# Kernel optimization log

Measured on AMD Instinct MI355X. Metric: run time of the kernel, lower is better.

Reference implementation:

```python
import jax, jax.numpy as jnp
import numpy as np

B, HGRID, WGRID = 4, 32, 32
L = 1 + HGRID * WGRID          # cls token + spatial tokens
INPUT_DIM = 512
HEAD_DIM = 512
N_HEAD = 8
QKV_DIM = HEAD_DIM * N_HEAD    # 4096


def pos_embed_2d(h, w, C, dtype):
    """Standard 2D sinusoidal positional embedding, shape (h*w, C)."""
    d = C // 4
    omega = 1.0 / (10000.0 ** (jnp.arange(d, dtype=jnp.float32) / d))
    ey = jnp.arange(h, dtype=jnp.float32)[:, None] * omega      # (h, d)
    ex = jnp.arange(w, dtype=jnp.float32)[:, None] * omega      # (w, d)
    emb_y = jnp.concatenate([jnp.sin(ey), jnp.cos(ey)], -1)     # (h, 2d)
    emb_x = jnp.concatenate([jnp.sin(ex), jnp.cos(ex)], -1)     # (w, 2d)
    emb = jnp.concatenate([
        jnp.broadcast_to(emb_y[:, None, :], (h, w, 2 * d)),
        jnp.broadcast_to(emb_x[None, :, :], (h, w, 2 * d)),
    ], -1)                                                       # (h, w, C)
    return emb.reshape(h * w, C).astype(dtype)


def setup_inputs() -> dict:
    key = jax.random.key(0)
    ks = jax.random.split(key, 16)
    s = 0.02
    inp = {
        "x": jax.random.normal(ks[0], (B, L, INPUT_DIM), dtype=jnp.float32),
        # Q/K/V linear: weight (out, in) as in torch Linear, bias zeros (per _init_bias)
        "Wq": jax.random.normal(ks[1], (QKV_DIM, INPUT_DIM), jnp.float32) * s,
        "bq": jnp.zeros((QKV_DIM,), jnp.float32),
        "Wk": jax.random.normal(ks[2], (QKV_DIM, INPUT_DIM), jnp.float32) * s,
        "bk": jnp.zeros((QKV_DIM,), jnp.float32),
        "Wv": jax.random.normal(ks[3], (QKV_DIM, INPUT_DIM), jnp.float32) * s,
        "bv": jnp.zeros((QKV_DIM,), jnp.float32),
        # 1x1 conv poolers: weight (out_ch, in_ch) = (HEAD_DIM, HEAD_DIM)
        "Wpq": jax.random.normal(ks[4], (HEAD_DIM, HEAD_DIM), jnp.float32) * s,
        "bpq": jax.random.normal(ks[5], (HEAD_DIM,), jnp.float32) * s,
        "Wpk": jax.random.normal(ks[6], (HEAD_DIM, HEAD_DIM), jnp.float32) * s,
        "bpk": jax.random.normal(ks[7], (HEAD_DIM,), jnp.float32) * s,
        "Wpv": jax.random.normal(ks[8], (HEAD_DIM, HEAD_DIM), jnp.float32) * s,
        "bpv": jax.random.normal(ks[9], (HEAD_DIM,), jnp.float32) * s,
        # dispatcher linear: (INPUT_DIM, QKV_DIM)
        "Wd": jax.random.normal(ks[10], (INPUT_DIM, QKV_DIM), jnp.float32) * s,
        "bd": jax.random.normal(ks[11], (INPUT_DIM,), jnp.float32) * s,
        "h": HGRID,
        "w": WGRID,
    }
    return inp


def _pool(t, Wp, bp):
    """AttentionPooler with kernel=1/stride=1: pointwise conv on spatial tokens,
    cls token passed through unchanged. t: (B, n_head, L, head_dim)."""
    cls_tok = t[:, :, :1, :]
    sp = jnp.einsum('bnlc,oc->bnlo', t[:, :, 1:, :], Wp) + bp
    return jnp.concatenate([cls_tok, sp], axis=2)


def reference(x, Wq, bq, Wk, bk, Wv, bv, Wpq, bpq, Wpk, bpk, Wpv, bpv, Wd, bd, h, w):
    Bs, Ls, _ = x.shape

    def proj(Wt, bt):
        y = jnp.einsum('bli,oi->blo', x, Wt) + bt
        return y.reshape(Bs, Ls, N_HEAD, HEAD_DIM).transpose(0, 2, 1, 3)  # (B,nh,L,hd)

    Q = proj(Wq, bq)
    K = proj(Wk, bk)
    V = proj(Wv, bv)

    PQ = _pool(Q, Wpq, bpq)
    PK = _pool(K, Wpk, bpk)
    PV = _pool(V, Wpv, bpv)

    # relative positional encoding added to pooled Q's spatial tokens
    emb = pos_embed_2d(h, w, HEAD_DIM, PQ.dtype)                 # (h*w, hd)
    PQ = jnp.concatenate([PQ[:, :, :1, :], PQ[:, :, 1:, :] + emb], axis=2)

    scale = 1.0 / jnp.sqrt(jnp.asarray(HEAD_DIM, PQ.dtype))
    logits = jnp.einsum('bnqc,bnkc->bnqk', PQ, PK) * scale
    attn = jax.nn.softmax(logits, axis=-1)
    sa = jnp.einsum('bnqk,bnkc->bnqc', attn, PV)

    # skip connection on spatial tokens only (cls row excluded)
    sa = jnp.concatenate([sa[:, :, :1, :], sa[:, :, 1:, :] + Q[:, :, 1:, :]], axis=2)

    stacked = sa.transpose(0, 2, 1, 3).reshape(Bs, Ls, QKV_DIM)
    out = jnp.einsum('blq,oq->blo', stacked, Wd) + bd
    return out
```

## Files before the change

kernel.cpp:

```cpp
#include <hip/hip_runtime.h>


typedef unsigned short u16;
typedef __attribute__((ext_vector_type(8))) short short8;
typedef __attribute__((ext_vector_type(4))) float floatx4;
typedef __attribute__((ext_vector_type(4))) unsigned short us4;

__device__ __forceinline__ u16 f2bf(float f) {
  union { float f; unsigned u; } x; x.f = f;
  unsigned r = (x.u + 0x7fffu + ((x.u >> 16) & 1u)) >> 16;
  return (u16)r;
}
__device__ __forceinline__ float bf2f(u16 u) {
  union { unsigned u; float f; } x; x.u = ((unsigned)u) << 16;
  return x.f;
}

__device__ __forceinline__ void gld_lds16(const void* g, void* l) {
  __builtin_amdgcn_global_load_lds(
      (const __attribute__((address_space(1))) void*)g,
      (__attribute__((address_space(3))) void*)l, 16, 0, 0);
}

struct CvtArgs { const float* src[8]; u16* dst[8]; int n4[8]; };

__global__ __launch_bounds__(256) void cvt_all(CvtArgs a, int total4, float* __restrict__ e) {
  int t = blockIdx.x * 256 + threadIdx.x;
  if (t >= total4) {
    int et = (t - total4) * 4;
    if (et >= 1024 * 512) return;
#pragma unroll
    for (int u = 0; u < 4; ++u) {
      int idx = et + u;
      int c = idx & 511, sp = idx >> 9;
      int y = sp >> 5, xg = sp & 31;
      int j = c & 127, seg = c >> 7;
      float omega = expf(-(float)j * (9.210340371976184f / 128.f));
      float arg = (float)((seg < 2) ? y : xg) * omega;
      e[idx] = (seg & 1) ? cosf(arg) : sinf(arg);
    }
    return;
  }
#pragma unroll
  for (int s = 0; s < 8; ++s) {
    if (t < a.n4[s]) {
      const float* sp = a.src[s] + (long)t * 4;
      u16* dp = a.dst[s] + (long)t * 4;
      float4 v = *(const float4*)sp;
      dp[0] = f2bf(v.x); dp[1] = f2bf(v.y); dp[2] = f2bf(v.z); dp[3] = f2bf(v.w);
      return;
    }
    t -= a.n4[s];
  }
}

__global__ __launch_bounds__(256) void cls_all(
    const u16* __restrict__ Q, const u16* __restrict__ K, const u16* __restrict__ V,
    u16* __restrict__ PQ, u16* __restrict__ PK, u16* __restrict__ PVt) {
  int t = blockIdx.x * 256 + threadIdx.x;
  int bn = t >> 9, c = t & 511;
  long o = (long)bn * 1025 * 512 + c;
  PQ[o] = Q[o];
  PK[o] = K[o];
  PVt[((long)bn * 512 + c) * 1088] = V[o];
}

__global__ __launch_bounds__(256) void s_edge(const u16* __restrict__ PQ,
                                              const u16* __restrict__ PK,
                                              u16* __restrict__ S, int nh) {
  int flat = blockIdx.x;
  int head, seg;
  if (nh == 32) {
    int xcd = flat & 7, s = flat >> 3;
    head = xcd + 8 * (s >> 2);
    seg = s & 3;
  } else {
    head = flat >> 2;
    seg = flat & 3;
  }
  const u16* pq = PQ + (long)head * 1025 * 512;
  const u16* pk = PK + (long)head * 1025 * 512;
  u16* sh = S + (long)head * 1025 * 1088;
#pragma unroll
  for (int i = 0; i < 3; ++i) {
    int local = i * 256 + (int)threadIdx.x;
    if (local >= 513) continue;
    int e = seg * 513 + local;
    if (e >= 2049) continue;
    int q, kv;
    if (e < 1025) { q = 1024; kv = e; }
    else { q = e - 1025; kv = 1024; }
    const u16* a = pq + (long)q * 512;
    const u16* b = pk + (long)kv * 512;
    float acc = 0.f;
    for (int k8 = 0; k8 < 64; ++k8) {
      short8 av = *(const short8*)(a + k8 * 8);
      short8 bv = *(const short8*)(b + k8 * 8);
#pragma unroll
      for (int u = 0; u < 8; ++u) acc += bf2f((u16)av[u]) * bf2f((u16)bv[u]);
    }
    sh[(long)q * 1088 + kv] = f2bf(acc * 0.04419417382415922f);
  }
}

__global__ __launch_bounds__(256) void softmax_rows(u16* __restrict__ S) {
  int flat = blockIdx.x;
  int xcd = flat & 7, s0 = flat >> 3;
  int zi = s0 / 257, blk = s0 - zi * 257;
  int head = xcd + 8 * zi;
  int wv = threadIdx.x >> 6, lane = threadIdx.x & 63;
  int row_i = blk * 4 + wv;
  if (row_i > 1024) return;
  u16* row = S + ((long)head * 1025 + row_i) * 1088;
  float v[16];
  float mx = -1e30f;
#pragma unroll
  for (int i = 0; i < 4; ++i) {
    us4 p = *(const us4*)(row + i * 256 + lane * 4);
#pragma unroll
    for (int e = 0; e < 4; ++e) { v[i * 4 + e] = bf2f(p[e]); mx = fmaxf(mx, v[i * 4 + e]); }
  }
  float e1024 = (lane == 0) ? bf2f(row[1024]) : -1e30f;
  mx = fmaxf(mx, e1024);
  for (int o = 32; o > 0; o >>= 1) mx = fmaxf(mx, __shfl_xor(mx, o, 64));
  float s = 0.f;
#pragma unroll
  for (int i = 0; i < 16; ++i) { v[i] = __expf(v[i] - mx); s += v[i]; }
  e1024 = (lane == 0) ? __expf(e1024 - mx) : 0.f;
  s += e1024;
  for (int o = 32; o > 0; o >>= 1) s += __shfl_xor(s, o, 64);
  float inv = 1.0f / s;
#pragma unroll
  for (int i = 0; i < 4; ++i) {
    us4 q;
#pragma unroll
    for (int e = 0; e < 4; ++e) q[e] = f2bf(v[i * 4 + e] * inv);
    *(us4*)(row + i * 256 + lane * 4) = q;
  }
  if (lane < 16) {
    us4 q;
#pragma unroll
    for (int e = 0; e < 4; ++e) q[e] = 0;
    if (lane == 0) q[0] = f2bf(e1024 * inv);
    *(us4*)(row + 1024 + lane * 4) = q;
  }
}

__global__ __launch_bounds__(256) void reduce2(const float* __restrict__ part,
                                               const float* __restrict__ bd,
                                               float* __restrict__ out) {
  int t = blockIdx.x * 256 + threadIdx.x;
  long i = (long)t * 4;
  const long STR = 4100ll * 512;
  float4 a = *(const float4*)(part + i);
  float4 b = *(const float4*)(part + i + STR);
  float4 bb = *(const float4*)(bd + (int)(i & 511));
  float4 r;
  r.x = a.x + b.x + bb.x;
  r.y = a.y + b.y + bb.y;
  r.z = a.z + b.z + bb.z;
  r.w = a.w + b.w + bb.w;
  *(float4*)(out + i) = r;
}

struct GP {
  const u16* A; const u16* A2; const u16* B; const u16* B2;
  const float* c0; const float* c1; const float* c2;
  const float* emb; const u16* resid;
  u16* o0; u16* o1; u16* o2;
  float* of; int bz0;
};

template <int MODE>
__global__ __launch_bounds__(256) void gemm_bt(GP g) {
  constexpr int KLEN = (MODE == 5) ? 2048 : ((MODE == 4) ? 1088 : 512);
  constexpr int KITER = KLEN / 64;
  constexpr bool LDSEP = (MODE == 0 || MODE == 1 || MODE == 3 || MODE == 4);
  __shared__ u16 smem[16384];
  u16* As = smem;
  u16* Bs = smem + 8192;
  const int tid = threadIdx.x;
  const int lane = tid & 63;
  const int wv = tid >> 6;
  const int wr = wv >> 1, wc = wv & 1;
  const int ccol = lane & 15;
  const int rgrp = lane >> 4;

  int mt, nt, bz;
  if constexpr (MODE == 3 || MODE == 4) {
    constexpr int PER = (MODE == 3) ? 64 : 36;
    constexpr int NTW = (MODE == 3) ? 8 : 4;
    int flat = blockIdx.x;
    int xcd = flat & 7, s = flat >> 3;
    bz = xcd + 8 * (s / PER);
    int tile = s % PER;
    mt = tile / NTW;
    nt = tile % NTW;
  } else if constexpr (MODE == 1) {
    int flat = blockIdx.x;
    int xcd = flat & 7, s = flat >> 3;
    bz = s >> 7;
    int rem = s & 127;
    mt = xcd * 32 + (rem >> 2);
    nt = rem & 3;
  } else if constexpr (MODE == 2) {
    int flat = blockIdx.x;
    int xcd = flat & 7, s = flat >> 3;
    bz = 0;
    mt = xcd * 32 + (s >> 2);
    nt = s & 3;
  } else {
    mt = blockIdx.y; nt = blockIdx.x; bz = blockIdx.z;
  }
  const int gbz = g.bz0 + bz;

  const u16* Ap = g.A;
  const u16* Bp = g.B;
  if constexpr (MODE == 1) {
    if (bz == 1) { Ap = g.A2; Bp = g.B2; }
  }

  int a_row[4], b_row[4], kx[4];
#pragma unroll
  for (int c = 0; c < 4; ++c) {
    int idx = c * 256 + tid;
    int row = idx >> 3;
    kx[c] = ((idx & 7) ^ (row & 7)) * 8;
    {
      int r = mt * 128 + row;
      int off;
      if constexpr (MODE == 0) { r = r < 4099 ? r : 4099; off = r * 512; }
      else if constexpr (MODE == 1 || MODE == 2) { off = ((r >> 10) * 1025 + 1 + (r & 1023)) * 512; }
      else if constexpr (MODE == 3) { off = gbz * (1025 * 512) + r * 512; }
      else if constexpr (MODE == 4) { r = r < 1024 ? r : 1024; off = bz * (1025 * 1088) + r * 1088; }
      else { r = r < 4099 ? r : 4099; off = r * 4096; }
      a_row[c] = off;
    }
    {
      int r = nt * 128 + row;
      int off;
      if constexpr (MODE == 3) { off = gbz * (1025 * 512) + r * 512; }
      else if constexpr (MODE == 4) { off = gbz * (512 * 1088) + r * 1088; }
      else if constexpr (MODE == 5) { off = r * 4096; }
      else { off = r * 512; }
      b_row[c] = off;
    }
  }

  floatx4 acc[4][4];
  {
    float binit[4] = {0.f, 0.f, 0.f, 0.f};
    if constexpr (MODE == 0) {
      int sec = nt >> 5;
      const float* bs = (sec == 0) ? g.c0 : (sec == 1) ? g.c1 : g.c2;
#pragma unroll
      for (int j = 0; j < 4; ++j) binit[j] = bs[(nt & 31) * 128 + wc * 64 + j * 16 + ccol];
    }
    if constexpr (MODE == 1) {
      const float* bs = bz ? g.c1 : g.c0;
#pragma unroll
      for (int j = 0; j < 4; ++j) binit[j] = bs[nt * 128 + wc * 64 + j * 16 + ccol];
    }
    if constexpr (MODE == 2) {
#pragma unroll
      for (int j = 0; j < 4; ++j) binit[j] = g.c0[nt * 128 + wc * 64 + j * 16 + ccol];
    }
#pragma unroll
    for (int i = 0; i < 4; ++i)
#pragma unroll
      for (int j = 0; j < 4; ++j)
#pragma unroll
        for (int rr = 0; rr < 4; ++rr) acc[i][j][rr] = binit[j];
  }

  const int kbase = (MODE == 5) ? bz * 2048 : 0;
  const int l15 = lane & 15;
  const int lq = lane >> 4;
  const int l7 = lane & 7;

  for (int kt = 0; kt < KITER; ++kt) {
    const int k0 = kbase + kt * 64;
#pragma unroll
    for (int c = 0; c < 4; ++c)
      gld_lds16(Ap + a_row[c] + k0 + kx[c], (char*)As + (c * 256 + wv * 64) * 16);
#pragma unroll
    for (int c = 0; c < 4; ++c)
      gld_lds16(Bp + b_row[c] + k0 + kx[c], (char*)Bs + (c * 256 + wv * 64) * 16);
    __syncthreads();
#pragma unroll
    for (int ks = 0; ks < 2; ++ks) {
      const int ch = ((ks * 4 + lq) ^ l7) * 8;
      short8 af[4], bf[4];
#pragma unroll
      for (int i = 0; i < 4; ++i)
        af[i] = *(const short8*)(As + (wr * 64 + i * 16 + l15) * 64 + ch);
#pragma unroll
      for (int j = 0; j < 4; ++j)
        bf[j] = *(const short8*)(Bs + (wc * 64 + j * 16 + l15) * 64 + ch);
#pragma unroll
      for (int i = 0; i < 4; ++i)
#pragma unroll
        for (int j = 0; j < 4; ++j)
          acc[i][j] = __builtin_amdgcn_mfma_f32_16x16x32_bf16(af[i], bf[j], acc[i][j], 0, 0, 0);
    }
    __syncthreads();
  }

  if constexpr (LDSEP) {
#pragma unroll
    for (int i = 0; i < 4; ++i)
#pragma unroll
      for (int j = 0; j < 4; ++j)
#pragma unroll
        for (int rr = 0; rr < 4; ++rr) {
          int lr = wr * 64 + i * 16 + rgrp * 4 + rr;
          int lc = wc * 64 + j * 16 + ccol;
          float v = acc[i][j][rr];
          if constexpr (MODE == 3) v *= 0.04419417382415922f;
          smem[lr * 128 + (lc ^ (rgrp << 4))] = f2bf(v);
        }
    __syncthreads();
#pragma unroll
    for (int q = 0; q < 8; ++q) {
      int cid = q * 256 + tid;
      int r = cid >> 4;
      int c = cid & 15;
      int pc = c ^ ((((unsigned)r >> 2) & 3) << 1);
      short8 val = *(const short8*)(smem + r * 128 + pc * 8);
      int grow = mt * 128 + r;
      if constexpr (MODE == 0) {
        if (grow < 4100) {
          int sec = nt >> 5;
          int col = (nt & 31) * 128 + c * 8;
          u16* ob = (sec == 0) ? g.o0 : (sec == 1) ? g.o1 : g.o2;
          int b = grow / 1025, l = grow - b * 1025;
          int n = col >> 9, ch2 = col & 511;
          *(short8*)(ob + ((long)(b * 8 + n) * 1025 + l) * 512 + ch2) = val;
        }
      } else if constexpr (MODE == 1) {
        int bn = grow >> 10, sp = grow & 1023;
        int gcol = nt * 128 + c * 8;
        short8 outv = val;
        if (bz == 0) {
          const float* ep = g.emb + sp * 512 + gcol;
          float4 e0 = *(const float4*)ep;
          float4 e1 = *(const float4*)(ep + 4);
          float ee[8] = {e0.x, e0.y, e0.z, e0.w, e1.x, e1.y, e1.z, e1.w};
#pragma unroll
          for (int e = 0; e < 8; ++e) outv[e] = (short)f2bf(bf2f((u16)val[e]) + ee[e]);
        }
        u16* dst = (bz == 0) ? g.o0 : g.o1;
        *(short8*)(dst + ((long)bn * 1025 + 1 + sp) * 512 + gcol) = outv;
      } else if constexpr (MODE == 3) {
        *(short8*)(g.o0 + ((long)bz * 1025 + grow) * 1088 + nt * 128 + c * 8) = val;
      } else {
        if (grow <= 1024) {
          int gcol0 = nt * 128 + c * 8;
          short8 outv = val;
          if (grow >= 1) {
            short8 rs = *(const short8*)(g.resid + ((long)gbz * 1025 + grow) * 512 + gcol0);
#pragma unroll
            for (int e = 0; e < 8; ++e)
              outv[e] = (short)f2bf(bf2f((u16)val[e]) + bf2f((u16)rs[e]));
          }
          int b = gbz >> 3, n = gbz & 7;
          *(short8*)(g.o0 + (((long)b * 1025 + grow) * 8 + n) * 512 + gcol0) = outv;
        }
      }
    }
  } else {
#pragma unroll
    for (int i = 0; i < 4; ++i) {
#pragma unroll
      for (int j = 0; j < 4; ++j) {
        const int gcol = nt * 128 + wc * 64 + j * 16 + ccol;
#pragma unroll
        for (int rr = 0; rr < 4; ++rr) {
          const int grow = mt * 128 + wr * 64 + i * 16 + rgrp * 4 + rr;
          float v = acc[i][j][rr];
          if constexpr (MODE == 2) {
            int bn = grow >> 10, sp = grow & 1023;
            g.o0[((long)bn * 512 + gcol) * 1088 + 1 + sp] = f2bf(v);
          } else {
            if (grow < 4100)
              g.of[((long)bz * 4100 + grow) * 512 + gcol] = v;
          }
        }
      }
    }
  }
}

extern "C" void kernel_launch(void* const* d_in, const int* in_sizes, int n_in,
                              void* d_out, int out_size, void* d_ws, size_t ws_size,
                              hipStream_t stream) {
  const float* x   = (const float*)d_in[0];
  const float* Wq  = (const float*)d_in[1];
  const float* bq  = (const float*)d_in[2];
  const float* Wk  = (const float*)d_in[3];
  const float* bk  = (const float*)d_in[4];
  const float* Wv  = (const float*)d_in[5];
  const float* bv  = (const float*)d_in[6];
  const float* Wpq = (const float*)d_in[7];
  const float* bpq = (const float*)d_in[8];
  const float* Wpk = (const float*)d_in[9];
  const float* bpk = (const float*)d_in[10];
  const float* Wpv = (const float*)d_in[11];
  const float* bpv = (const float*)d_in[12];
  const float* Wd  = (const float*)d_in[13];
  const float* bd  = (const float*)d_in[14];
  float* out = (float*)d_out;

  char* ws = (char*)d_ws;
  size_t off = 0;
  auto alloc = [&](size_t bytes) {
    char* p = ws + off;
    off += (bytes + 255) & ~(size_t)255;
    return p;
  };
  u16* Wpqb = (u16*)alloc(512ull * 512 * 2);
  u16* Wpkb = (u16*)alloc(512ull * 512 * 2);
  u16* Wpvb = (u16*)alloc(512ull * 512 * 2);
  u16* Wdb  = (u16*)alloc(4096ull * 512 * 2);
  u16* Q    = (u16*)alloc(32ull * 1025 * 512 * 2);
  u16* PQ   = (u16*)alloc(32ull * 1025 * 512 * 2);
  u16* PK   = (u16*)alloc(32ull * 1025 * 512 * 2);
  u16* PVt  = (u16*)alloc(32ull * 512 * 1088 * 2);
  size_t s_off = off;
  u16* K    = (u16*)alloc(32ull * 1025 * 512 * 2);
  u16* V    = (u16*)alloc(32ull * 1025 * 512 * 2);
  u16* xb   = (u16*)alloc(4100ull * 512 * 2);
  u16* Wqb  = (u16*)alloc(4096ull * 512 * 2);
  u16* Wkb  = (u16*)alloc(4096ull * 512 * 2);
  u16* Wvb  = (u16*)alloc(4096ull * 512 * 2);
  float* embp = (float*)alloc(1024ull * 512 * 4);
  size_t fixed_need = off;
  u16* S = (u16*)(ws + s_off);
  float* part = (float*)PQ;
  (void)in_sizes; (void)n_in; (void)out_size;

  const size_t sbytes = 1025ull * 1088 * 2;
  size_t need1 = s_off + 32ull * sbytes;
  size_t need2 = s_off + 16ull * sbytes;
  size_t stk4_off = s_off + ((8ull * sbytes + 255) & ~(size_t)255);
  size_t need4 = stk4_off + 4100ull * 4096 * 2;
  int nchunk;
  u16* stk;
  if (ws_size >= need1)      { nchunk = 1; stk = PK; }
  else if (ws_size >= need2 && ws_size >= fixed_need) { nchunk = 2; stk = PK; }
  else if (ws_size >= need4 && ws_size >= fixed_need) {
    nchunk = 4; stk = (u16*)(ws + stk4_off);
  } else return;
  if (nchunk == 2) {
    size_t stk2_off = s_off + ((16ull * sbytes + 255) & ~(size_t)255);
    if (ws_size >= stk2_off + 4100ull * 4096 * 2) stk = (u16*)(ws + stk2_off);
    else {
      nchunk = 4;
      if (ws_size >= need4) stk = (u16*)(ws + stk4_off);
      else return;
    }
  }
  int hpc = 32 / nchunk;

  CvtArgs ca;
  ca.src[0] = x;   ca.dst[0] = xb;   ca.n4[0] = 4100 * 512 / 4;
  ca.src[1] = Wq;  ca.dst[1] = Wqb;  ca.n4[1] = 4096 * 512 / 4;
  ca.src[2] = Wk;  ca.dst[2] = Wkb;  ca.n4[2] = 4096 * 512 / 4;
  ca.src[3] = Wv;  ca.dst[3] = Wvb;  ca.n4[3] = 4096 * 512 / 4;
  ca.src[4] = Wpq; ca.dst[4] = Wpqb; ca.n4[4] = 512 * 512 / 4;
  ca.src[5] = Wpk; ca.dst[5] = Wpkb; ca.n4[5] = 512 * 512 / 4;
  ca.src[6] = Wpv; ca.dst[6] = Wpvb; ca.n4[6] = 512 * 512 / 4;
  ca.src[7] = Wd;  ca.dst[7] = Wdb;  ca.n4[7] = 512 * 4096 / 4;
  int total4 = 0;
  for (int s = 0; s < 8; ++s) total4 += ca.n4[s];
  int grid1 = (total4 + 1024 * 512 / 4 + 255) / 256;
  cvt_all<<<grid1, 256, 0, stream>>>(ca, total4, embp);

  {
    GP g = {};
    g.A = xb; g.B = Wqb;
    g.c0 = bq; g.c1 = bk; g.c2 = bv;
    g.o0 = Q; g.o1 = K; g.o2 = V;
    gemm_bt<0><<<dim3(96, 33, 1), 256, 0, stream>>>(g);
  }

  cls_all<<<(32 * 512) / 256, 256, 0, stream>>>(Q, K, V, PQ, PK, PVt);

  {
    GP g = {};
    g.A = Q; g.A2 = K; g.B = Wpqb; g.B2 = Wpkb;
    g.c0 = bpq; g.c1 = bpk; g.emb = embp;
    g.o0 = PQ; g.o1 = PK;
    gemm_bt<1><<<dim3(2048, 1, 1), 256, 0, stream>>>(g);
  }
  {
    GP g = {};
    g.A = V; g.B = Wpvb; g.c0 = bpv; g.o0 = PVt;
    gemm_bt<2><<<dim3(1024, 1, 1), 256, 0, stream>>>(g);
  }

  for (int c = 0; c < nchunk; ++c) {
    GP g3 = {}; g3.A = PQ; g3.B = PK; g3.o0 = S; g3.bz0 = c * hpc;
    gemm_bt<3><<<dim3(64 * hpc, 1, 1), 256, 0, stream>>>(g3);
    s_edge<<<hpc * 4, 256, 0, stream>>>(
        PQ + (long)c * hpc * 1025 * 512, PK + (long)c * hpc * 1025 * 512, S, hpc);
    softmax_rows<<<257 * hpc, 256, 0, stream>>>(S);
    GP g4 = {}; g4.A = S; g4.B = PVt; g4.resid = Q; g4.o0 = stk; g4.bz0 = c * hpc;
    gemm_bt<4><<<dim3(36 * hpc, 1, 1), 256, 0, stream>>>(g4);
  }

  {
    GP g = {}; g.A = stk; g.B = Wdb; g.of = part;
    gemm_bt<5><<<dim3(4, 33, 2), 256, 0, stream>>>(g);
  }
  reduce2<<<(4100 * 512 / 4 + 255) / 256, 256, 0, stream>>>(part, bd, out);
}
```

Measured before the change: 463.9 us.

## Move cls token to end of pooled tensors, fuse cls copy, coalesce PVt stores

Pooled Q/K/V now keep spatial tokens at rows 0..1023 and the cls token at row 1024, with the cls rows written directly from the QKV projection epilogue, so the separate cls_all kernel is removed. The MODE 2 pooled-V epilogue now transposes through swizzled shared memory and writes coalesced 16-byte stores into PVt instead of scattered 2-byte stores. The output epilogue remaps row 1024 back to token 0. s_edge is split into 8 segments per head instead of 4 to raise parallelism. This adds index remapping complexity and a few strided scalar writes for the cls column of PVt.

```diff
diff --git a/kernel.cpp b/kernel.cpp
--- a/kernel.cpp
+++ b/kernel.cpp
@@ -54,17 +54,6 @@
   }
 }
 
-__global__ __launch_bounds__(256) void cls_all(
-    const u16* __restrict__ Q, const u16* __restrict__ K, const u16* __restrict__ V,
-    u16* __restrict__ PQ, u16* __restrict__ PK, u16* __restrict__ PVt) {
-  int t = blockIdx.x * 256 + threadIdx.x;
-  int bn = t >> 9, c = t & 511;
-  long o = (long)bn * 1025 * 512 + c;
-  PQ[o] = Q[o];
-  PK[o] = K[o];
-  PVt[((long)bn * 512 + c) * 1088] = V[o];
-}
-
 __global__ __launch_bounds__(256) void s_edge(const u16* __restrict__ PQ,
                                               const u16* __restrict__ PK,
                                               u16* __restrict__ S, int nh) {
@@ -72,20 +61,20 @@
   int head, seg;
   if (nh == 32) {
     int xcd = flat & 7, s = flat >> 3;
-    head = xcd + 8 * (s >> 2);
-    seg = s & 3;
+    head = xcd + 8 * (s >> 3);
+    seg = s & 7;
   } else {
-    head = flat >> 2;
-    seg = flat & 3;
+    head = flat >> 3;
+    seg = flat & 7;
   }
   const u16* pq = PQ + (long)head * 1025 * 512;
   const u16* pk = PK + (long)head * 1025 * 512;
   u16* sh = S + (long)head * 1025 * 1088;
 #pragma unroll
-  for (int i = 0; i < 3; ++i) {
+  for (int i = 0; i < 2; ++i) {
     int local = i * 256 + (int)threadIdx.x;
-    if (local >= 513) continue;
-    int e = seg * 513 + local;
+    if (local >= 257) continue;
+    int e = seg * 257 + local;
     if (e >= 2049) continue;
     int q, kv;
     if (e < 1025) { q = 1024; kv = e; }
@@ -168,6 +157,7 @@
   const float* c0; const float* c1; const float* c2;
   const float* emb; const u16* resid;
   u16* o0; u16* o1; u16* o2;
+  u16* p0; u16* p1; u16* p2;
   float* of; int bz0;
 };
 
@@ -335,7 +325,17 @@
           u16* ob = (sec == 0) ? g.o0 : (sec == 1) ? g.o1 : g.o2;
           int b = grow / 1025, l = grow - b * 1025;
           int n = col >> 9, ch2 = col & 511;
-          *(short8*)(ob + ((long)(b * 8 + n) * 1025 + l) * 512 + ch2) = val;
+          long bn = (long)b * 8 + n;
+          *(short8*)(ob + (bn * 1025 + l) * 512 + ch2) = val;
+          if (l == 0) {
+            if (sec == 0) *(short8*)(g.p0 + (bn * 1025 + 1024) * 512 + ch2) = val;
+            else if (sec == 1) *(short8*)(g.p1 + (bn * 1025 + 1024) * 512 + ch2) = val;
+            else {
+#pragma unroll
+              for (int e = 0; e < 8; ++e)
+                g.p2[(bn * 512 + ch2 + e) * 1088 + 1024] = (u16)val[e];
+            }
+          }
         }
       } else if constexpr (MODE == 1) {
         int bn = grow >> 10, sp = grow & 1023;
@@ -350,24 +350,50 @@
           for (int e = 0; e < 8; ++e) outv[e] = (short)f2bf(bf2f((u16)val[e]) + ee[e]);
         }
         u16* dst = (bz == 0) ? g.o0 : g.o1;
-        *(short8*)(dst + ((long)bn * 1025 + 1 + sp) * 512 + gcol) = outv;
+        *(short8*)(dst + ((long)bn * 1025 + sp) * 512 + gcol) = outv;
       } else if constexpr (MODE == 3) {
         *(short8*)(g.o0 + ((long)bz * 1025 + grow) * 1088 + nt * 128 + c * 8) = val;
       } else {
         if (grow <= 1024) {
           int gcol0 = nt * 128 + c * 8;
           short8 outv = val;
-          if (grow >= 1) {
-            short8 rs = *(const short8*)(g.resid + ((long)gbz * 1025 + grow) * 512 + gcol0);
+          int l = (grow == 1024) ? 0 : grow + 1;
+          if (grow < 1024) {
+            short8 rs = *(const short8*)(g.resid + ((long)gbz * 1025 + l) * 512 + gcol0);
 #pragma unroll
             for (int e = 0; e < 8; ++e)
               outv[e] = (short)f2bf(bf2f((u16)val[e]) + bf2f((u16)rs[e]));
           }
           int b = gbz >> 3, n = gbz & 7;
-          *(short8*)(g.o0 + (((long)b * 1025 + grow) * 8 + n) * 512 + gcol0) = outv;
+          *(short8*)(g.o0 + (((long)b * 1025 + l) * 8 + n) * 512 + gcol0) = outv;
         }
       }
     }
+  } else if constexpr (MODE == 2) {
+#pragma unroll
+    for (int i = 0; i < 4; ++i)
+#pragma unroll
+      for (int j = 0; j < 4; ++j)
+#pragma unroll
+        for (int rr = 0; rr < 4; ++rr) {
+          int lr2 = wc * 64 + j * 16 + ccol;
+          int lc2 = wr * 64 + i * 16 + rgrp * 4 + rr;
+          smem[lr2 * 128 + (lc2 ^ ((lr2 & 15) << 3))] = f2bf(acc[i][j][rr]);
+        }
+    __syncthreads();
+    {
+      int bn = mt >> 3, sp0 = (mt & 7) * 128;
+#pragma unroll
+      for (int q = 0; q < 8; ++q) {
+        int cid = q * 256 + tid;
+        int r = cid >> 4;
+        int c = cid & 15;
+        int pc = c ^ (r & 15);
+        short8 val = *(const short8*)(smem + r * 128 + pc * 8);
+        int ch = nt * 128 + r;
+        *(short8*)(g.o0 + ((long)(bn * 512 + ch)) * 1088 + sp0 + c * 8) = val;
+      }
+    }
   } else {
 #pragma unroll
     for (int i = 0; i < 4; ++i) {
@@ -377,14 +403,8 @@
 #pragma unroll
         for (int rr = 0; rr < 4; ++rr) {
           const int grow = mt * 128 + wr * 64 + i * 16 + rgrp * 4 + rr;
-          float v = acc[i][j][rr];
-          if constexpr (MODE == 2) {
-            int bn = grow >> 10, sp = grow & 1023;
-            g.o0[((long)bn * 512 + gcol) * 1088 + 1 + sp] = f2bf(v);
-          } else {
-            if (grow < 4100)
-              g.of[((long)bz * 4100 + grow) * 512 + gcol] = v;
-          }
+          if (grow < 4100)
+            g.of[((long)bz * 4100 + grow) * 512 + gcol] = acc[i][j][rr];
         }
       }
     }
@@ -481,10 +501,9 @@
     g.A = xb; g.B = Wqb;
     g.c0 = bq; g.c1 = bk; g.c2 = bv;
     g.o0 = Q; g.o1 = K; g.o2 = V;
+    g.p0 = PQ; g.p1 = PK; g.p2 = PVt;
     gemm_bt<0><<<dim3(96, 33, 1), 256, 0, stream>>>(g);
   }
-
-  cls_all<<<(32 * 512) / 256, 256, 0, stream>>>(Q, K, V, PQ, PK, PVt);
 
   {
     GP g = {};
@@ -502,7 +521,7 @@
   for (int c = 0; c < nchunk; ++c) {
     GP g3 = {}; g3.A = PQ; g3.B = PK; g3.o0 = S; g3.bz0 = c * hpc;
     gemm_bt<3><<<dim3(64 * hpc, 1, 1), 256, 0, stream>>>(g3);
-    s_edge<<<hpc * 4, 256, 0, stream>>>(
+    s_edge<<<hpc * 8, 256, 0, stream>>>(
         PQ + (long)c * hpc * 1025 * 512, PK + (long)c * hpc * 1025 * 512, S, hpc);
     softmax_rows<<<257 * hpc, 256, 0, stream>>>(S);
     GP g4 = {}; g4.A = S; g4.B = PVt; g4.resid = Q; g4.o0 = stk; g4.bz0 = c * hpc;
```

After: 446.7 us. 3.7% less time.
